# Kernel optimization log

Hardware: AMD Instinct MI355X
Metric: run time of the kernel (lower is better)

## Reference

```python
import jax, jax.numpy as jnp
import numpy as np

EPS = 1e-6  # nn.PairwiseDistance default eps (added to the difference)


def setup_inputs() -> dict:
    key = jax.random.key(0)
    feature = jax.random.normal(key, (16384, 256), dtype=jnp.float32)
    return {"feature": feature}


def reference(feature) -> jnp.ndarray:
    n = feature.shape[0]
    # all-pairs inner products [n, n]
    dots = jnp.matmul(feature, feature.T)
    # mask self-similarity on the diagonal with -1 (as in the torch code)
    dots = dots.at[jnp.diag_indices(n)].set(-1.0)
    # row-wise nearest neighbor (argmax of inner product)
    I = jnp.argmax(dots, axis=1)  # [n] int
    # PairwiseDistance(p=2): ||x1 - x2 + eps||_2
    diff = feature - feature[I] + EPS  # [n, d]
    distances = jnp.sqrt(jnp.sum(diff * diff, axis=1))  # [n]
    loss_uniform = -jnp.mean(jnp.log(n * distances))
    return loss_uniform
```

## Files before the change

kernel.cpp:

```cpp
#include <hip/hip_runtime.h>
#include <hip/hip_bf16.h>
#include <math.h>


#define NROWS 16384
#define DIM   256
#define BM    128
#define BN    128
#define EPSF  1e-6f

typedef __attribute__((ext_vector_type(8))) __bf16 bf16x8;
typedef __attribute__((ext_vector_type(4))) float f32x4;

typedef const __attribute__((address_space(1))) void* gas1_t;
typedef __attribute__((address_space(3))) void* las3_t;

__device__ __forceinline__ void glds16(const void* g, void* l) {
    __builtin_amdgcn_global_load_lds((gas1_t)g, (las3_t)l, 16, 0, 0);
}

__device__ __forceinline__ unsigned short f2bf(float f) {
    union { float f; unsigned u; } x; x.f = f;
    const unsigned u = x.u;
    return (unsigned short)((u + 0x7FFFu + ((u >> 16) & 1u)) >> 16);
}

__device__ __forceinline__ unsigned umax2(unsigned a, unsigned b) {
    return a > b ? a : b;
}

__global__ __launch_bounds__(256)
void convert_kernel(const float* __restrict__ F, unsigned short* __restrict__ Fb,
                    unsigned long long* __restrict__ packed,
                    unsigned long long* __restrict__ scratch)
{
    const int t = blockIdx.x * 256 + threadIdx.x;
    const float4 a = *reinterpret_cast<const float4*>(F + (size_t)t * 8);
    const float4 b = *reinterpret_cast<const float4*>(F + (size_t)t * 8 + 4);
    ushort4 lo, hi;
    lo.x = f2bf(a.x); lo.y = f2bf(a.y); lo.z = f2bf(a.z); lo.w = f2bf(a.w);
    hi.x = f2bf(b.x); hi.y = f2bf(b.y); hi.z = f2bf(b.z); hi.w = f2bf(b.w);
    *reinterpret_cast<ushort4*>(Fb + (size_t)t * 8)     = lo;
    *reinterpret_cast<ushort4*>(Fb + (size_t)t * 8 + 4) = hi;
    if (t < NROWS) packed[t] = 0ull;
    #pragma unroll
    for (int q = 0; q < 4; ++q)
        scratch[(size_t)t * 4 + q] = 0ull;
}

__global__ __launch_bounds__(256, 2)
void mfma_sym_kernel(const unsigned short* __restrict__ Fb,
                     unsigned long long* __restrict__ packed,
                     unsigned long long* __restrict__ scratch)
{
    __shared__ __align__(16) unsigned short As[BM * DIM];
    __shared__ __align__(16) unsigned short Bs[2 * 4096];

    const int tid  = threadIdx.x;
    const int w    = tid >> 6;
    const int l    = tid & 63;
    const int rs   = (int)blockIdx.x >> 3;
    const int ck   = (int)blockIdx.x & 7;
    const int span = 128 - rs;
    const int t0   = rs + (span * ck) / 8;
    const int t1   = rs + (span * (ck + 1)) / 8;
    if (t0 >= t1) return;

    const int row0 = rs * BM;
    const int wrow = (w >> 1) * 64;
    const int wcol = (w & 1) * 64;
    const int lc   = l & 15;
    const int lr4  = l >> 4;

    {
        const int lr = l >> 5;
        const int sc = (l & 31) ^ (2 * w + lr);
        #pragma unroll
        for (int q = 0; q < 16; ++q)
            glds16(Fb + (size_t)(row0 + 8 * q + 2 * w + lr) * DIM + sc * 8,
                   &As[(q * 4 + w) * 512]);
    }

    const int bsc = (l & 3) ^ ((l >> 3) & 3);
    const int bco = l >> 2;

    #pragma unroll
    for (int q = 0; q < 2; ++q)
        glds16(Fb + (size_t)(t0 * BM + q * 64 + w * 16 + bco) * DIM + bsc * 8,
               &Bs[q * 2048 + w * 512]);

    f32x4 acc[4][4];
    #pragma unroll
    for (int i = 0; i < 4; ++i)
        #pragma unroll
        for (int j = 0; j < 4; ++j)
            acc[i][j] = (f32x4){512.f, 512.f, 512.f, 512.f};

    unsigned best[4][4] = {};

    for (int t = t0; t < t1; ++t) {
        const bool dt = (t == rs);
        #pragma unroll
        for (int kq = 0; kq < 8; ++kq) {
            __syncthreads();

            const int nt = (kq < 7) ? t : t + 1;
            const int nk = (kq < 7) ? (kq + 1) * 32 : 0;
            if (nt < t1) {
                #pragma unroll
                for (int q = 0; q < 2; ++q)
                    glds16(Fb + (size_t)(nt * BM + q * 64 + w * 16 + bco) * DIM
                               + nk + bsc * 8,
                           &Bs[((kq & 1) ^ 1) * 4096 + q * 2048 + w * 512]);
            }

            const int rbase = (kq & 1) * 4096;
            bf16x8 afv[4], bfv[4];
            #pragma unroll
            for (int i = 0; i < 4; ++i) {
                const int r = wrow + i * 16 + lc;
                const int g = kq * 4 + lr4;
                afv[i] = *reinterpret_cast<const bf16x8*>(
                    &As[r * 256 + ((g ^ (r & 7)) << 3)]);
            }
            #pragma unroll
            for (int j = 0; j < 4; ++j) {
                const int c = wcol + j * 16 + lc;
                const int p = lr4 ^ ((c >> 1) & 3);
                bfv[j] = *reinterpret_cast<const bf16x8*>(
                    &Bs[rbase + c * 32 + p * 8]);
            }
            #pragma unroll
            for (int j = 0; j < 4; ++j)
                #pragma unroll
                for (int i = 0; i < 4; ++i)
                    acc[i][j] = __builtin_amdgcn_mfma_f32_16x16x32_bf16(
                        afv[i], bfv[j], acc[i][j], 0, 0, 0);
        }

        #pragma unroll
        for (int j = 0; j < 4; ++j) {
            unsigned kb = 0u;
            #pragma unroll
            for (int i = 0; i < 4; ++i)
                #pragma unroll
                for (int g = 0; g < 4; ++g) {
                    const int r_loc = wrow + i * 16 + lr4 * 4 + g;
                    unsigned key = (__float_as_uint(acc[i][j][g]) & 0xFFFFF800u)
                                   | (unsigned)(127 - r_loc);
                    if (dt && (wcol + j * 16 + lc == r_loc)) key = 0u;
                    kb = umax2(kb, key);
                }
            kb = umax2(kb, (unsigned)__shfl_xor((int)kb, 16));
            kb = umax2(kb, (unsigned)__shfl_xor((int)kb, 32));
            if (lr4 == 0) {
                const unsigned grow = (unsigned)row0 + (127u - (kb & 0x7FFu));
                const unsigned long long pk =
                    ((unsigned long long)(kb & 0xFFFFF800u) << 32) |
                    (0xFFFFFFFFu - grow);
                atomicMax(&scratch[((size_t)t * 128 + rs) * 128
                                   + wcol + j * 16 + lc], pk);
            }
        }

        const int tl = t - t0;
        unsigned cb[4];
        #pragma unroll
        for (int j = 0; j < 4; ++j)
            cb[j] = 2047u - (unsigned)(tl * 128 + wcol + j * 16 + lc);

        if (dt) {
            #pragma unroll
            for (int i = 0; i < 4; ++i)
                #pragma unroll
                for (int g = 0; g < 4; ++g) {
                    const int r_loc = wrow + i * 16 + lr4 * 4 + g;
                    unsigned bk = best[i][g];
                    #pragma unroll
                    for (int j = 0; j < 4; ++j) {
                        unsigned key = (__float_as_uint(acc[i][j][g])
                                        & 0xFFFFF800u) | cb[j];
                        if (wcol + j * 16 + lc == r_loc) key = 0u;
                        bk = umax2(bk, key);
                        acc[i][j][g] = 512.f;
                    }
                    best[i][g] = bk;
                }
        } else {
            #pragma unroll
            for (int i = 0; i < 4; ++i)
                #pragma unroll
                for (int g = 0; g < 4; ++g) {
                    const unsigned k0 = (__float_as_uint(acc[i][0][g]) & 0xFFFFF800u) | cb[0];
                    const unsigned k1 = (__float_as_uint(acc[i][1][g]) & 0xFFFFF800u) | cb[1];
                    const unsigned k2 = (__float_as_uint(acc[i][2][g]) & 0xFFFFF800u) | cb[2];
                    const unsigned k3 = (__float_as_uint(acc[i][3][g]) & 0xFFFFF800u) | cb[3];
                    best[i][g] = umax2(best[i][g],
                                       umax2(umax2(k0, k1), umax2(k2, k3)));
                    acc[i][0][g] = 512.f; acc[i][1][g] = 512.f;
                    acc[i][2][g] = 512.f; acc[i][3][g] = 512.f;
                }
        }
    }

    #pragma unroll
    for (int i = 0; i < 4; ++i)
        #pragma unroll
        for (int g = 0; g < 4; ++g) {
            unsigned key = best[i][g];
            #pragma unroll
            for (int m = 8; m >= 1; m >>= 1)
                key = umax2(key, (unsigned)__shfl_xor((int)key, m));
            if (lc == 0) {
                const int r = row0 + wrow + i * 16 + lr4 * 4 + g;
                const unsigned c = (unsigned)(t0 * BM) + (2047u - (key & 0x7FFu));
                const unsigned long long pk =
                    ((unsigned long long)(key & 0xFFFFF800u) << 32) |
                    (0xFFFFFFFFu - c);
                atomicMax(&packed[r], pk);
            }
        }
}

__global__ __launch_bounds__(256)
void dist_loss_kernel(const float* __restrict__ F,
                      const unsigned long long* __restrict__ packed,
                      const unsigned long long* __restrict__ scratch,
                      double* __restrict__ partials)
{
    const int tid  = threadIdx.x;
    const int lane = tid & 63;
    const int w    = tid >> 6;
    const int gw   = blockIdx.x * 4 + w;
    double local = 0.0;
    for (int r = gw; r < NROWS; r += 1024) {
        const int tR = r >> 7;
        const int cl = r & 127;
        unsigned long long best = packed[r];
        const unsigned long long* base = scratch + (size_t)tR * 16384 + cl;
        if (lane <= tR) {
            unsigned long long v = base[(size_t)lane * 128];
            if (lane + 64 <= tR) {
                const unsigned long long v2 = base[(size_t)(lane + 64) * 128];
                if (v2 > v) v = v2;
            }
            if (v > best) best = v;
        }
        #pragma unroll
        for (int m = 32; m >= 1; m >>= 1) {
            const unsigned long long o = __shfl_xor(best, m);
            if (o > best) best = o;
        }
        const int idx = (int)(0xFFFFFFFFu - (unsigned)(best & 0xFFFFFFFFull));

        const float4 a = *reinterpret_cast<const float4*>(
            F + (size_t)r * DIM + (lane << 2));
        const float4 b = *reinterpret_cast<const float4*>(
            F + (size_t)idx * DIM + (lane << 2));
        const float dx = a.x - b.x + EPSF;
        const float dy = a.y - b.y + EPSF;
        const float dz = a.z - b.z + EPSF;
        const float dw = a.w - b.w + EPSF;
        float ss = dx * dx + dy * dy + dz * dz + dw * dw;
        #pragma unroll
        for (int m = 32; m >= 1; m >>= 1) ss += __shfl_xor(ss, m);
        if (lane == 0)
            local += 0.5 * log((double)ss) + log((double)NROWS);
    }
    __shared__ double sm[4];
    if (lane == 0) sm[w] = local;
    __syncthreads();
    if (tid == 0) partials[blockIdx.x] = sm[0] + sm[1] + sm[2] + sm[3];
}

__global__ __launch_bounds__(256)
void finalize_kernel(const double* __restrict__ partials, float* __restrict__ out)
{
    const int tid = threadIdx.x;
    double v = partials[tid];
    #pragma unroll
    for (int m = 32; m >= 1; m >>= 1) v += __shfl_xor(v, m);
    __shared__ double sm[4];
    if ((tid & 63) == 0) sm[tid >> 6] = v;
    __syncthreads();
    if (tid == 0) out[0] = (float)(-(sm[0] + sm[1] + sm[2] + sm[3]) / (double)NROWS);
}

extern "C" void kernel_launch(void* const* d_in, const int* in_sizes, int n_in,
                              void* d_out, int out_size, void* d_ws, size_t ws_size,
                              hipStream_t stream)
{
    const float* F   = (const float*)d_in[0];
    float*       out = (float*)d_out;

    char* ws = (char*)d_ws;
    unsigned short*     Fb       = (unsigned short*)ws;
    unsigned long long* packed   = (unsigned long long*)(ws + 8388608);
    unsigned long long* scratch  = (unsigned long long*)(ws + 8519680);
    double*             partials = (double*)(ws + 25296896);

    convert_kernel<<<2048, 256, 0, stream>>>(F, Fb, packed, scratch);
    mfma_sym_kernel<<<(NROWS / BM) * 8, 256, 0, stream>>>(Fb, packed, scratch);
    dist_loss_kernel<<<256, 256, 0, stream>>>(F, packed, scratch, partials);
    finalize_kernel<<<1, 256, 0, stream>>>(partials, out);
}
```

Before: 126.5 us.

## Switch all-pairs Gram matmul from bf16 to fp8 e4m3 MFMA

Converts features to fp8 e4m3 instead of bf16 and computes the symmetric Gram tiles with the 16x16x32 fp8 MFMA. The LDS layout is rebuilt around 16-byte k-chunks per row, and occupancy is raised to three blocks per CU. The aim is to halve operand bytes and use the faster fp8 matrix rate. The risk is that fp8 rounding changes which neighbour wins the argmax, especially for near-tied candidates, which would alter the loss. The new LDS layout also drops the XOR swizzle, which could introduce bank conflicts.

```diff
diff --git a/kernel.cpp b/kernel.cpp
--- a/kernel.cpp
+++ b/kernel.cpp
@@ -9,7 +9,6 @@
 #define BN    128
 #define EPSF  1e-6f
 
-typedef __attribute__((ext_vector_type(8))) __bf16 bf16x8;
 typedef __attribute__((ext_vector_type(4))) float f32x4;
 
 typedef const __attribute__((address_space(1))) void* gas1_t;
@@ -19,42 +18,52 @@
     __builtin_amdgcn_global_load_lds((gas1_t)g, (las3_t)l, 16, 0, 0);
 }
 
-__device__ __forceinline__ unsigned short f2bf(float f) {
-    union { float f; unsigned u; } x; x.f = f;
-    const unsigned u = x.u;
-    return (unsigned short)((u + 0x7FFFu + ((u >> 16) & 1u)) >> 16);
-}
-
 __device__ __forceinline__ unsigned umax2(unsigned a, unsigned b) {
     return a > b ? a : b;
 }
 
+__device__ __forceinline__ unsigned f2e4m3(float f) {
+    union { float f; unsigned u; } x; x.f = f;
+    const unsigned s = (x.u >> 24) & 0x80u;
+    const unsigned au = x.u & 0x7FFFFFFFu;
+    float af = __uint_as_float(au);
+    if (au < 0x3B800000u) {
+        const int q = (int)(af * 512.0f + 0.5f);
+        return s | (unsigned)q;
+    }
+    const unsigned add = 0x7FFFFu + ((au >> 20) & 1u);
+    const unsigned v = au + add;
+    const unsigned e = (v >> 23) - 120u;
+    return s | (e << 3) | ((v >> 20) & 7u);
+}
+
 __global__ __launch_bounds__(256)
-void convert_kernel(const float* __restrict__ F, unsigned short* __restrict__ Fb,
+void convert_kernel(const float* __restrict__ F, unsigned char* __restrict__ F8,
                     unsigned long long* __restrict__ packed,
                     unsigned long long* __restrict__ scratch)
 {
     const int t = blockIdx.x * 256 + threadIdx.x;
     const float4 a = *reinterpret_cast<const float4*>(F + (size_t)t * 8);
     const float4 b = *reinterpret_cast<const float4*>(F + (size_t)t * 8 + 4);
-    ushort4 lo, hi;
-    lo.x = f2bf(a.x); lo.y = f2bf(a.y); lo.z = f2bf(a.z); lo.w = f2bf(a.w);
-    hi.x = f2bf(b.x); hi.y = f2bf(b.y); hi.z = f2bf(b.z); hi.w = f2bf(b.w);
-    *reinterpret_cast<ushort4*>(Fb + (size_t)t * 8)     = lo;
-    *reinterpret_cast<ushort4*>(Fb + (size_t)t * 8 + 4) = hi;
+    const unsigned lo = f2e4m3(a.x) | (f2e4m3(a.y) << 8) |
+                        (f2e4m3(a.z) << 16) | (f2e4m3(a.w) << 24);
+    const unsigned hi = f2e4m3(b.x) | (f2e4m3(b.y) << 8) |
+                        (f2e4m3(b.z) << 16) | (f2e4m3(b.w) << 24);
+    uint2 v; v.x = lo; v.y = hi;
+    *reinterpret_cast<uint2*>(F8 + (size_t)t * 8) = v;
     if (t < NROWS) packed[t] = 0ull;
     #pragma unroll
     for (int q = 0; q < 4; ++q)
         scratch[(size_t)t * 4 + q] = 0ull;
 }
 
-__global__ __launch_bounds__(256, 2)
-void mfma_sym_kernel(const unsigned short* __restrict__ Fb,
-                     unsigned long long* __restrict__ packed,
-                     unsigned long long* __restrict__ scratch)
-{
-    __shared__ __align__(16) unsigned short As[BM * DIM];
-    __shared__ __align__(16) unsigned short Bs[2 * 4096];
+__global__ __launch_bounds__(256, 3)
+void mfma_sym_fp8_kernel(const unsigned char* __restrict__ F8,
+                         unsigned long long* __restrict__ packed,
+                         unsigned long long* __restrict__ scratch)
+{
+    __shared__ __align__(16) unsigned char As[32768];
+    __shared__ __align__(16) unsigned char Bs[2 * 8192];
 
     const int tid  = threadIdx.x;
     const int w    = tid >> 6;
@@ -72,22 +81,22 @@
     const int lc   = l & 15;
     const int lr4  = l >> 4;
 
-    {
-        const int lr = l >> 5;
-        const int sc = (l & 31) ^ (2 * w + lr);
-        #pragma unroll
-        for (int q = 0; q < 16; ++q)
-            glds16(Fb + (size_t)(row0 + 8 * q + 2 * w + lr) * DIM + sc * 8,
-                   &As[(q * 4 + w) * 512]);
-    }
-
-    const int bsc = (l & 3) ^ ((l >> 3) & 3);
-    const int bco = l >> 2;
-
-    #pragma unroll
-    for (int q = 0; q < 2; ++q)
-        glds16(Fb + (size_t)(t0 * BM + q * 64 + w * 16 + bco) * DIM + bsc * 8,
-               &Bs[q * 2048 + w * 512]);
+    #pragma unroll
+    for (int m = 0; m < 8; ++m) {
+        const int q   = 8 * w + m;
+        const int k16 = q >> 1;
+        const int row = (q & 1) * 64 + l;
+        glds16(F8 + (size_t)(row0 + row) * DIM + k16 * 16, &As[q * 1024]);
+    }
+
+    #pragma unroll
+    for (int q2 = 0; q2 < 2; ++q2) {
+        const int col = q2 * 64 + l;
+        glds16(F8 + (size_t)(t0 * BM + col) * DIM + w * 16,
+               &Bs[(2 * w + q2) * 1024]);
+    }
+
+    const long* __restrict__ Al = reinterpret_cast<const long*>(As);
 
     f32x4 acc[4][4];
     #pragma unroll
@@ -98,44 +107,50 @@
 
     unsigned best[4][4] = {};
 
+    const int k16r = (lr4 >> 1);
+    const int odd  = lr4 & 1;
+
     for (int t = t0; t < t1; ++t) {
         const bool dt = (t == rs);
         #pragma unroll
-        for (int kq = 0; kq < 8; ++kq) {
+        for (int ss = 0; ss < 4; ++ss) {
             __syncthreads();
 
-            const int nt = (kq < 7) ? t : t + 1;
-            const int nk = (kq < 7) ? (kq + 1) * 32 : 0;
+            const int nt  = (ss < 3) ? t : t + 1;
+            const int nss = (ss < 3) ? ss + 1 : 0;
             if (nt < t1) {
                 #pragma unroll
-                for (int q = 0; q < 2; ++q)
-                    glds16(Fb + (size_t)(nt * BM + q * 64 + w * 16 + bco) * DIM
-                               + nk + bsc * 8,
-                           &Bs[((kq & 1) ^ 1) * 4096 + q * 2048 + w * 512]);
-            }
-
-            const int rbase = (kq & 1) * 4096;
-            bf16x8 afv[4], bfv[4];
-            #pragma unroll
-            for (int i = 0; i < 4; ++i) {
-                const int r = wrow + i * 16 + lc;
-                const int g = kq * 4 + lr4;
-                afv[i] = *reinterpret_cast<const bf16x8*>(
-                    &As[r * 256 + ((g ^ (r & 7)) << 3)]);
-            }
-            #pragma unroll
-            for (int j = 0; j < 4; ++j) {
-                const int c = wcol + j * 16 + lc;
-                const int p = lr4 ^ ((c >> 1) & 3);
-                bfv[j] = *reinterpret_cast<const bf16x8*>(
-                    &Bs[rbase + c * 32 + p * 8]);
-            }
-            #pragma unroll
-            for (int j = 0; j < 4; ++j)
-                #pragma unroll
-                for (int i = 0; i < 4; ++i)
-                    acc[i][j] = __builtin_amdgcn_mfma_f32_16x16x32_bf16(
-                        afv[i], bfv[j], acc[i][j], 0, 0, 0);
+                for (int q2 = 0; q2 < 2; ++q2) {
+                    const int col = q2 * 64 + l;
+                    glds16(F8 + (size_t)(nt * BM + col) * DIM + nss * 64 + w * 16,
+                           &Bs[((ss & 1) ^ 1) * 8192 + (2 * w + q2) * 1024]);
+                }
+            }
+
+            const long* __restrict__ Bl =
+                reinterpret_cast<const long*>(Bs) + (ss & 1) * 1024;
+
+            #pragma unroll
+            for (int h = 0; h < 2; ++h) {
+                const int kk = h * 2 + k16r;
+                long afv[4], bfv[4];
+                #pragma unroll
+                for (int i = 0; i < 4; ++i) {
+                    const int r = wrow + i * 16 + lc;
+                    afv[i] = Al[(ss * 4 + kk) * 256 + r * 2 + odd];
+                }
+                #pragma unroll
+                for (int j = 0; j < 4; ++j) {
+                    const int c = wcol + j * 16 + lc;
+                    bfv[j] = Bl[kk * 256 + c * 2 + odd];
+                }
+                #pragma unroll
+                for (int j = 0; j < 4; ++j)
+                    #pragma unroll
+                    for (int i = 0; i < 4; ++i)
+                        acc[i][j] = __builtin_amdgcn_mfma_f32_16x16x32_fp8_fp8(
+                            afv[i], bfv[j], acc[i][j], 0, 0, 0);
+            }
         }
 
         #pragma unroll
@@ -294,13 +309,13 @@
     float*       out = (float*)d_out;
 
     char* ws = (char*)d_ws;
-    unsigned short*     Fb       = (unsigned short*)ws;
-    unsigned long long* packed   = (unsigned long long*)(ws + 8388608);
-    unsigned long long* scratch  = (unsigned long long*)(ws + 8519680);
-    double*             partials = (double*)(ws + 25296896);
-
-    convert_kernel<<<2048, 256, 0, stream>>>(F, Fb, packed, scratch);
-    mfma_sym_kernel<<<(NROWS / BM) * 8, 256, 0, stream>>>(Fb, packed, scratch);
+    unsigned char*      F8       = (unsigned char*)ws;
+    unsigned long long* packed   = (unsigned long long*)(ws + 4194304);
+    unsigned long long* scratch  = (unsigned long long*)(ws + 4325376);
+    double*             partials = (double*)(ws + 21102592);
+
+    convert_kernel<<<2048, 256, 0, stream>>>(F, F8, packed, scratch);
+    mfma_sym_fp8_kernel<<<(NROWS / BM) * 8, 256, 0, stream>>>(F8, packed, scratch);
     dist_loss_kernel<<<256, 256, 0, stream>>>(F, packed, scratch, partials);
     finalize_kernel<<<1, 256, 0, stream>>>(partials, out);
 }
```

New measurement: 106.7 us. 15.6% less time.
